# Kernel optimization log

Hardware: AMD Instinct MI355X
Metric: run time of the kernel (lower is better)

The kernel has to match this reference:

```python
import jax, jax.numpy as jnp
import numpy as np

B, T, D, H = 2, 1024, 1024, 16
HS = D // H
EPS = 1e-5
SCALE = float(np.sqrt(HS))  # faithful bug: scores / hs**(-0.5) == scores * sqrt(hs)


def setup_inputs() -> dict:
    key = jax.random.key(0)
    ks = jax.random.split(key, 20)
    n = lambda k, shape: jax.random.normal(k, shape, dtype=jnp.float32) * 0.02
    return {
        "src": jax.random.normal(ks[0], (B, T, D), dtype=jnp.float32),
        "att": jax.random.normal(ks[1], (B, T, D), dtype=jnp.float32),
        # causal masked self-attention (no biases on q/k/v)
        "wq_m": n(ks[2], (H, D, HS)), "wk_m": n(ks[3], (H, D, HS)), "wv_m": n(ks[4], (H, D, HS)),
        "proj_m_w": n(ks[5], (D, D)), "proj_m_b": jnp.zeros((D,), jnp.float32),
        # final (cross) attention (biases on q/k/v)
        "wq_f": n(ks[6], (H, D, HS)), "wk_f": n(ks[7], (H, D, HS)), "wv_f": n(ks[8], (H, D, HS)),
        "bq_f": jnp.zeros((H, HS), jnp.float32), "bk_f": jnp.zeros((H, HS), jnp.float32),
        "bv_f": jnp.zeros((H, HS), jnp.float32),
        "proj_f_w": n(ks[9], (D, D)), "proj_f_b": jnp.zeros((D,), jnp.float32),
        # FFN
        "w1": n(ks[10], (D, 4 * D)), "b1": jnp.zeros((4 * D,), jnp.float32),
        "w2": n(ks[11], (4 * D, D)), "b2": jnp.zeros((D,), jnp.float32),
        # shared RMSNorm weight (one instance reused at all three sites)
        "norm_w": jnp.ones((D,), jnp.float32),
    }


def rmsnorm(x, w):
    return x * jax.lax.rsqrt(jnp.mean(x * x, axis=-1, keepdims=True) + EPS) * w


def masked_attn(x, wq, wk, wv):
    q = jnp.einsum('btd,hde->bhte', x, wq)
    k = jnp.einsum('btd,hde->bhte', x, wk)
    v = jnp.einsum('btd,hde->bhte', x, wv)
    scores = jnp.einsum('bhte,bhse->bhts', q, k) * SCALE  # [B,H,T,T]
    causal = jnp.tril(jnp.ones((T, T), dtype=bool))
    scores = jnp.where(causal, scores, -jnp.inf)
    a = jax.nn.softmax(scores, axis=-1)
    o = jnp.einsum('bhts,bhse->bhte', a, v)
    return o.transpose(0, 2, 1, 3).reshape(B, T, D)  # concat heads


def final_attn(x, att, wq, bq, wk, bk, wv, bv):
    q = jnp.einsum('btd,hde->bhte', att, wq) + bq[None, :, None, :]
    k = jnp.einsum('btd,hde->bhte', att, wk) + bk[None, :, None, :]
    v = jnp.einsum('btd,hde->bhte', x, wv) + bv[None, :, None, :]
    scores = jnp.einsum('bhte,bhse->bhts', q, k) * SCALE
    a = jax.nn.softmax(scores, axis=-1)
    o = jnp.einsum('bhts,bhse->bhte', a, v)
    return o.transpose(0, 2, 1, 3).reshape(B, T, D)


def reference(src, att, wq_m, wk_m, wv_m, proj_m_w, proj_m_b,
              wq_f, wk_f, wv_f, bq_f, bk_f, bv_f, proj_f_w, proj_f_b,
              w1, b1, w2, b2, norm_w):
    # masked self-attention block
    m = masked_attn(rmsnorm(src, norm_w), wq_m, wk_m, wv_m)
    m_out = src + (m @ proj_m_w + proj_m_b)
    # cross attention block (q/k from norm(att), v from m_out)
    f = final_attn(m_out, rmsnorm(att, norm_w), wq_f, bq_f, wk_f, bk_f, wv_f, bv_f)
    f_out = m_out + (f @ proj_f_w + proj_f_b)
    # FFN block
    h = rmsnorm(f_out, norm_w)
    h = jax.nn.gelu(h @ w1 + b1, approximate=False) @ w2 + b2
    return f_out + h
```

## Files before the change

### kernel.cpp

```cpp
#include <hip/hip_runtime.h>
#include <math.h>

#define BB 2
#define TT 1024
#define DD 1024
#define HH 16
#define HS 64
#define NROWS (BB*TT)

typedef _Float16 f16;
typedef __attribute__((ext_vector_type(8))) _Float16 half8;
typedef __attribute__((ext_vector_type(4))) _Float16 half4;
typedef __attribute__((ext_vector_type(4))) float f32x4;

constexpr float EPS   = 1e-5f;
constexpr float SCALE = 8.0f;

__device__ __forceinline__ void load_lds16(const f16* g, f16* l) {
    __builtin_amdgcn_global_load_lds(
        (const __attribute__((address_space(1))) unsigned int*)g,
        (__attribute__((address_space(3))) unsigned int*)l, 16, 0, 0);
}

__device__ __forceinline__ int xcd_swizzle(int lin, int total) {
    if ((total & 7) == 0) {
        const int chunk = total >> 3;
        lin = (lin & 7) * chunk + (lin >> 3);
    }
    return lin;
}

__global__ __launch_bounds__(256) void prologue_all(
    const float* __restrict__ wq_m, const float* __restrict__ wk_m,
    const float* __restrict__ wv_m, const float* __restrict__ proj_m_w,
    const float* __restrict__ wq_f, const float* __restrict__ wk_f,
    const float* __restrict__ wv_f, const float* __restrict__ proj_f_w,
    const float* __restrict__ w1,   const float* __restrict__ w2,
    f16* __restrict__ wt,
    const float* __restrict__ bq, const float* __restrict__ bk,
    float* __restrict__ biascat,
    const float* __restrict__ src, const float* __restrict__ att,
    const float* __restrict__ normw,
    f16* __restrict__ xn_s, f16* __restrict__ xn_a)
{
    const int bid = blockIdx.x;
    const int tid = threadIdx.x;
    const size_t M_ = 1024 * 1024;

    __shared__ float tt[64][65];

    if (bid == 4096) {
        for (int j = tid; j < 5120; j += 256)
            biascat[j] = (j < 3072) ? 0.f : ((j < 4096) ? bq[j - 3072] : bk[j - 4096]);
        return;
    }

    if (bid > 4096) {
        const int rrow = bid - 4097;
        const int row  = rrow & (NROWS - 1);
        const float* xr = ((rrow < NROWS) ? src : att) + (size_t)row * DD;
        f16* out = ((rrow < NROWS) ? xn_s : xn_a) + (size_t)row * DD;

        float4 xv = reinterpret_cast<const float4*>(xr)[tid];
        float ss = xv.x*xv.x + xv.y*xv.y + xv.z*xv.z + xv.w*xv.w;
        float* red = &tt[0][0];
        red[tid] = ss; __syncthreads();
        for (int s = 128; s > 0; s >>= 1) {
            if (tid < s) red[tid] += red[tid + s];
            __syncthreads();
        }
        const float inv = rsqrtf(red[0] * (1.0f / DD) + EPS);
        float4 wv = reinterpret_cast<const float4*>(normw)[tid];
        half4 o;
        o.x = (f16)(xv.x * inv * wv.x);
        o.y = (f16)(xv.y * inv * wv.y);
        o.z = (f16)(xv.z * inv * wv.z);
        o.w = (f16)(xv.w * inv * wv.w);
        *reinterpret_cast<half4*>(&out[tid * 4]) = o;
        return;
    }

    const float* W; f16* Wt; int K, N, lognk, t; bool headw;
    if (bid < 768)       { const int m = bid >> 8;
                           W = (m == 0) ? wq_m : (m == 1) ? wk_m : wv_m;
                           Wt = wt + (size_t)m * M_;
                           K = 1024; N = 1024; lognk = 4; headw = true;  t = bid & 255; }
    else if (bid < 1024) { W = proj_m_w; Wt = wt + 6 * M_;
                           K = 1024; N = 1024; lognk = 4; headw = false; t = bid - 768; }
    else if (bid < 1792) { const int m = (bid - 1024) >> 8;
                           W = (m == 0) ? wq_f : (m == 1) ? wk_f : wv_f;
                           Wt = wt + (size_t)(3 + m) * M_;
                           K = 1024; N = 1024; lognk = 4; headw = true;  t = (bid - 1024) & 255; }
    else if (bid < 2048) { W = proj_f_w; Wt = wt + 7 * M_;
                           K = 1024; N = 1024; lognk = 4; headw = false; t = bid - 1792; }
    else if (bid < 3072) { W = w1; Wt = wt + 8 * M_;
                           K = 1024; N = 4096; lognk = 4; headw = false; t = bid - 2048; }
    else                 { W = w2; Wt = wt + 12 * M_;
                           K = 4096; N = 1024; lognk = 6; headw = false; t = bid - 3072; }

    const int k0 = (t & ((1 << lognk) - 1)) * 64;
    const int n0 = (t >> lognk) * 64;

    #pragma unroll
    for (int r = 0; r < 4; ++r) {
        const int idx = tid + r * 256;
        const int kl  = idx >> 4;
        const int nl4 = (idx & 15) * 4;
        const float* gp;
        if (headw) {
            gp = W + ((size_t)(n0 >> 6) * K + (k0 + kl)) * 64 + nl4;
        } else {
            gp = W + (size_t)(k0 + kl) * N + n0 + nl4;
        }
        float4 v = *reinterpret_cast<const float4*>(gp);
        tt[kl][nl4 + 0] = v.x; tt[kl][nl4 + 1] = v.y;
        tt[kl][nl4 + 2] = v.z; tt[kl][nl4 + 3] = v.w;
    }
    __syncthreads();
    #pragma unroll
    for (int r = 0; r < 4; ++r) {
        const int idx = tid + r * 256;
        const int nl  = idx >> 4;
        const int kl4 = (idx & 15) * 4;
        half4 o;
        o.x = (f16)tt[kl4 + 0][nl];
        o.y = (f16)tt[kl4 + 1][nl];
        o.z = (f16)tt[kl4 + 2][nl];
        o.w = (f16)tt[kl4 + 3][nl];
        *reinterpret_cast<half4*>(&Wt[(size_t)(n0 + nl) * K + k0 + kl4]) = o;
    }
}

template<int BM, int EPI, bool HEADOUT, bool SPLITA, bool OHALF, bool PARTIAL>
__global__ __launch_bounds__(256, 2) void gemm_mfma(
    const f16* __restrict__ A1,
    const f16* __restrict__ A2,
    const f16* __restrict__ Bt,
    const float* __restrict__ bias,
    float* __restrict__ outF,
    f16* __restrict__ outH,
    int N, int K, int splitN)
{
    constexpr int BK = 32;
    constexpr int MI = 4;
    constexpr int NI = (BM == 128) ? 4 : 2;
    constexpr int WN = (BM == 128) ? 64 : 32;
    constexpr int ASLOT = BM * 4;
    constexpr int AINST = ASLOT / 256;

    __shared__ f16 ldsA[2][ASLOT * 8];
    __shared__ f16 ldsB[2][512 * 8];

    const int tid  = threadIdx.x;
    const int lane = tid & 63;
    const int wid  = tid >> 6;
    const int gy = gridDim.y;
    const int lin = xcd_swizzle(blockIdx.y * gridDim.x + blockIdx.x,
                                gridDim.x * gy);
    const int m0 = (lin % gy) * BM;
    const int n0 = (lin / gy) * 128;
    const int wm = (BM == 128) ? (wid >> 1) : 0;
    const int wn = (BM == 128) ? (wid & 1) : wid;

    const int Klen  = K / gridDim.z;
    const int kbase = blockIdx.z * Klen;

    const f16* Aptr = (SPLITA && n0 >= splitN) ? A2 : A1;

    f32x4 acc[MI][NI];
    #pragma unroll
    for (int i = 0; i < MI; ++i)
        #pragma unroll
        for (int j = 0; j < NI; ++j)
            acc[i][j] = (f32x4){0.f, 0.f, 0.f, 0.f};

    auto stage = [&](int buf, int kt) {
        const int k0 = kbase + kt * BK;
        #pragma unroll
        for (int i = 0; i < AINST; ++i) {
            const int s   = (wid * AINST + i) * 64 + lane;
            const int kh  = s / BM;
            const int row = s % BM;
            load_lds16(Aptr + (size_t)(m0 + row) * K + (k0 + kh * 8),
                       &ldsA[buf][s * 8]);
        }
        #pragma unroll
        for (int i = 0; i < 2; ++i) {
            const int s   = (wid * 2 + i) * 64 + lane;
            const int kh  = s >> 7;
            const int col = s & 127;
            load_lds16(Bt + (size_t)(n0 + col) * K + (k0 + kh * 8),
                       &ldsB[buf][s * 8]);
        }
    };

    const int NT = Klen / BK;
    stage(0, 0);
    __syncthreads();
    int cur = 0;
    const int l15 = lane & 15, l4 = lane >> 4;
    for (int kt = 0; kt < NT; ++kt) {
        if (kt + 1 < NT) stage(cur ^ 1, kt + 1);
        half8 af[MI], bfr[NI];
        #pragma unroll
        for (int mi = 0; mi < MI; ++mi)
            af[mi] = *reinterpret_cast<const half8*>(
                &ldsA[cur][(l4 * BM + wm * 64 + mi * 16 + l15) * 8]);
        #pragma unroll
        for (int ni = 0; ni < NI; ++ni)
            bfr[ni] = *reinterpret_cast<const half8*>(
                &ldsB[cur][(l4 * 128 + wn * WN + ni * 16 + l15) * 8]);
        #pragma unroll
        for (int mi = 0; mi < MI; ++mi)
            #pragma unroll
            for (int ni = 0; ni < NI; ++ni)
                acc[mi][ni] = __builtin_amdgcn_mfma_f32_16x16x32_f16(
                    af[mi], bfr[ni], acc[mi][ni], 0, 0, 0);
        __syncthreads();
        cur ^= 1;
    }

    f16* pout = nullptr;
    if (PARTIAL) {
        const size_t MN = (size_t)gridDim.y * BM * N;
        pout = outH + (size_t)blockIdx.z * MN;
    }

    #pragma unroll
    for (int mi = 0; mi < MI; ++mi) {
        #pragma unroll
        for (int ni = 0; ni < NI; ++ni) {
            #pragma unroll
            for (int r = 0; r < 4; ++r) {
                const int row = m0 + wm * 64 + mi * 16 + l4 * 4 + r;
                const int col = n0 + wn * WN + ni * 16 + l15;
                float v = acc[mi][ni][r];
                if (PARTIAL) {
                    pout[(size_t)row * N + col] = (f16)v;
                    continue;
                }
                if (EPI >= 1) v += bias[col];
                if (EPI == 2) v = 0.5f * v * (1.0f + erff(v * 0.70710678118f));
                size_t oidx;
                if (HEADOUT) {
                    const int mat = col >> 10;
                    const int h = (col >> 6) & 15, e = col & 63;
                    const int b = row >> 10, t = row & (TT - 1);
                    oidx = (size_t)mat * ((size_t)NROWS * DD)
                         + ((size_t)((b * HH + h) * TT + t)) * HS + e;
                } else {
                    oidx = (size_t)row * N + col;
                }
                if (OHALF) outH[oidx] = (f16)v;
                else       outF[oidx] = v;
            }
        }
    }
}

template<int MODE>
__global__ __launch_bounds__(256) void reduce_fuse(const f16* __restrict__ part,
                                                   const float* __restrict__ bias,
                                                   const float* __restrict__ residF,
                                                   const f16* __restrict__ residH,
                                                   float* __restrict__ outF,
                                                   f16* __restrict__ outH,
                                                   const float* __restrict__ normw,
                                                   f16* __restrict__ xnout) {
    const size_t MN  = (size_t)NROWS * 1024;
    const int tid = threadIdx.x;
    const size_t idx = ((size_t)blockIdx.x * 256 + tid) * 4;
    float o[4];
    {
        half4 p0 = *reinterpret_cast<const half4*>(part + idx);
        half4 p1 = *reinterpret_cast<const half4*>(part + MN + idx);
        half4 p2 = *reinterpret_cast<const half4*>(part + 2 * MN + idx);
        half4 p3 = *reinterpret_cast<const half4*>(part + 3 * MN + idx);
        float4 bi = *reinterpret_cast<const float4*>(bias + (idx & 1023));
        o[0] = (float)p0.x + (float)p1.x + (float)p2.x + (float)p3.x + bi.x;
        o[1] = (float)p0.y + (float)p1.y + (float)p2.y + (float)p3.y + bi.y;
        o[2] = (float)p0.z + (float)p1.z + (float)p2.z + (float)p3.z + bi.z;
        o[3] = (float)p0.w + (float)p1.w + (float)p2.w + (float)p3.w + bi.w;
    }
    if (MODE == 0 || MODE == 2) {
        float4 rs = *reinterpret_cast<const float4*>(residF + idx);
        o[0] += rs.x; o[1] += rs.y; o[2] += rs.z; o[3] += rs.w;
    } else {
        half4 rh = *reinterpret_cast<const half4*>(residH + idx);
        o[0] += (float)rh.x; o[1] += (float)rh.y; o[2] += (float)rh.z; o[3] += (float)rh.w;
    }

    if (MODE == 0) {
        half4 h;
        h.x = (f16)o[0]; h.y = (f16)o[1]; h.z = (f16)o[2]; h.w = (f16)o[3];
        *reinterpret_cast<half4*>(outH + idx) = h;
        return;
    }

    float4 ov = {o[0], o[1], o[2], o[3]};
    *reinterpret_cast<float4*>(outF + idx) = ov;

    if (MODE == 1) {
        __shared__ float red[256];
        red[tid] = o[0]*o[0] + o[1]*o[1] + o[2]*o[2] + o[3]*o[3];
        __syncthreads();
        for (int s = 128; s > 0; s >>= 1) {
            if (tid < s) red[tid] += red[tid + s];
            __syncthreads();
        }
        const float inv = rsqrtf(red[0] * (1.0f / DD) + EPS);
        float4 nw = *reinterpret_cast<const float4*>(normw + (idx & 1023));
        half4 h;
        h.x = (f16)(o[0] * inv * nw.x);
        h.y = (f16)(o[1] * inv * nw.y);
        h.z = (f16)(o[2] * inv * nw.z);
        h.w = (f16)(o[3] * inv * nw.w);
        *reinterpret_cast<half4*>(xnout + idx) = h;
    }
}

__global__ __launch_bounds__(256) void reduce_vf(const f16* __restrict__ part,
                                                 const float* __restrict__ bv,
                                                 f16* __restrict__ out) {
    const size_t MN = (size_t)NROWS * 1024;
    const int t   = blockIdx.x;
    const int tid = threadIdx.x;
    const int n   = tid * 4;
    const size_t idx = (size_t)t * 1024 + n;
    half4 p0 = *reinterpret_cast<const half4*>(part + idx);
    half4 p1 = *reinterpret_cast<const half4*>(part + MN + idx);
    float4 bi = *reinterpret_cast<const float4*>(bv + n);
    half4 o;
    o.x = (f16)((float)p0.x + (float)p1.x + bi.x);
    o.y = (f16)((float)p0.y + (float)p1.y + bi.y);
    o.z = (f16)((float)p0.z + (float)p1.z + bi.z);
    o.w = (f16)((float)p0.w + (float)p1.w + bi.w);
    const int b = t >> 10, tl = t & (TT - 1);
    const int h = n >> 6, e = n & (HS - 1);
    *reinterpret_cast<half4*>(
        &out[((size_t)(b * HH + h) * TT + tl) * HS + e]) = o;
}

template<bool CAUSAL>
__global__ __launch_bounds__(256) void attn_mfma(const f16* __restrict__ Q,
                                                 const f16* __restrict__ Kg,
                                                 const f16* __restrict__ Vg,
                                                 f16* __restrict__ O) {
    int iq, bh;
    if (CAUSAL) {
        bh = blockIdx.y;
        iq = (blockIdx.y < 16) ? blockIdx.x : (15 - blockIdx.x);
    } else {
        iq = blockIdx.x; bh = blockIdx.y;
    }
    const int tid = threadIdx.x;
    const int lane = tid & 63;
    const int w   = tid >> 6;
    const int l15 = lane & 15, l4 = lane >> 4;

    __shared__ f16 Ks[512 * 8];
    __shared__ f16 VT[64 * 72];
    __shared__ f16 Ps[4][16 * 72];

    const f16* qb = Q  + ((size_t)bh * TT + (size_t)iq * 64) * HS;
    const f16* kb = Kg + (size_t)bh * TT * HS;
    const f16* vb = Vg + (size_t)bh * TT * HS;

    half8 qf[2];
    #pragma unroll
    for (int ks = 0; ks < 2; ++ks)
        qf[ks] = *reinterpret_cast<const half8*>(
            qb + (size_t)(w * 16 + l15) * HS + ks * 32 + l4 * 8);

    f32x4 oacc[4];
    #pragma unroll
    for (int ni = 0; ni < 4; ++ni) oacc[ni] = (f32x4){0.f, 0.f, 0.f, 0.f};
    float m_run[4], l_run[4];
    #pragma unroll
    for (int r = 0; r < 4; ++r) { m_run[r] = -1e30f; l_run[r] = 0.f; }

    const int sp  = lane & 31;
    const int ehv = lane >> 5;
    const int c0  = w * 16 + ehv * 8;

    const int ntiles = CAUSAL ? (iq + 1) : (TT / 64);
    for (int js = 0; js < ntiles; ++js) {
        __syncthreads();

        #pragma unroll
        for (int i = 0; i < 2; ++i) {
            const int slot = (w * 2 + i) * 64 + lane;
            load_lds16(kb + (size_t)(js * 64 + (slot & 63)) * HS + (slot >> 6) * 8,
                       &Ks[slot * 8]);
        }
        {
            const f16* vrow = vb + (size_t)(js * 64 + 2 * sp) * HS + c0;
            uint4 r0 = *reinterpret_cast<const uint4*>(vrow);
            uint4 r1 = *reinterpret_cast<const uint4*>(vrow + HS);
            const unsigned rc0[4] = {r0.x, r0.y, r0.z, r0.w};
            const unsigned rc1[4] = {r1.x, r1.y, r1.z, r1.w};
            #pragma unroll
            for (int i = 0; i < 8; ++i) {
                const unsigned lo = (i & 1) ? (rc0[i >> 1] >> 16) : (rc0[i >> 1] & 0xffffu);
                const unsigned hi = (i & 1) ? (rc1[i >> 1] >> 16) : (rc1[i >> 1] & 0xffffu);
                *reinterpret_cast<unsigned*>(&VT[(c0 + i) * 72 + 2 * sp]) = lo | (hi << 16);
            }
        }
        __syncthreads();

        f32x4 sacc[4];
        #pragma unroll
        for (int ni = 0; ni < 4; ++ni) sacc[ni] = (f32x4){0.f, 0.f, 0.f, 0.f};
        __builtin_amdgcn_s_setprio(1);
        #pragma unroll
        for (int ks = 0; ks < 2; ++ks) {
            #pragma unroll
            for (int ni = 0; ni < 4; ++ni) {
                half8 kf = *reinterpret_cast<const half8*>(
                    &Ks[((ks * 4 + l4) * 64 + ni * 16 + l15) * 8]);
                sacc[ni] = __builtin_amdgcn_mfma_f32_16x16x32_f16(qf[ks], kf, sacc[ni], 0, 0, 0);
            }
        }
        __builtin_amdgcn_s_setprio(0);

        float sv[4][4];
        #pragma unroll
        for (int ni = 0; ni < 4; ++ni) {
            #pragma unroll
            for (int r = 0; r < 4; ++r) {
                float x = sacc[ni][r] * SCALE;
                if (CAUSAL && js == iq) {
                    const int sg = js * 64 + ni * 16 + l15;
                    const int qg = iq * 64 + w * 16 + l4 * 4 + r;
                    if (sg > qg) x = -1e30f;
                }
                sv[ni][r] = x;
            }
        }

        #pragma unroll
        for (int r = 0; r < 4; ++r) {
            float rm = fmaxf(fmaxf(sv[0][r], sv[1][r]), fmaxf(sv[2][r], sv[3][r]));
            rm = fmaxf(rm, __shfl_xor(rm, 1));
            rm = fmaxf(rm, __shfl_xor(rm, 2));
            rm = fmaxf(rm, __shfl_xor(rm, 4));
            rm = fmaxf(rm, __shfl_xor(rm, 8));
            const float mnew = fmaxf(m_run[r], rm);
            const float corr = __expf(m_run[r] - mnew);
            float p0 = __expf(sv[0][r] - mnew);
            float p1 = __expf(sv[1][r] - mnew);
            float p2 = __expf(sv[2][r] - mnew);
            float p3 = __expf(sv[3][r] - mnew);
            float sum = p0 + p1 + p2 + p3;
            sum += __shfl_xor(sum, 1);
            sum += __shfl_xor(sum, 2);
            sum += __shfl_xor(sum, 4);
            sum += __shfl_xor(sum, 8);
            l_run[r] = l_run[r] * corr + sum;
            m_run[r] = mnew;
            #pragma unroll
            for (int ni = 0; ni < 4; ++ni) oacc[ni][r] *= corr;
            f16* prow = &Ps[w][(l4 * 4 + r) * 72];
            prow[ 0 + l15] = (f16)p0;
            prow[16 + l15] = (f16)p1;
            prow[32 + l15] = (f16)p2;
            prow[48 + l15] = (f16)p3;
        }

        __builtin_amdgcn_s_setprio(1);
        #pragma unroll
        for (int ks = 0; ks < 2; ++ks) {
            half8 pf = *reinterpret_cast<const half8*>(&Ps[w][l15 * 72 + ks * 32 + l4 * 8]);
            #pragma unroll
            for (int ni = 0; ni < 4; ++ni) {
                half8 vf = *reinterpret_cast<const half8*>(
                    &VT[(ni * 16 + l15) * 72 + ks * 32 + l4 * 8]);
                oacc[ni] = __builtin_amdgcn_mfma_f32_16x16x32_f16(pf, vf, oacc[ni], 0, 0, 0);
            }
        }
        __builtin_amdgcn_s_setprio(0);
    }

    const int b = bh >> 4, h = bh & (HH - 1);
    #pragma unroll
    for (int r = 0; r < 4; ++r) {
        const float inv = 1.0f / l_run[r];
        const int t = iq * 64 + w * 16 + l4 * 4 + r;
        #pragma unroll
        for (int ni = 0; ni < 4; ++ni)
            O[((size_t)(b * TT + t)) * DD + h * HS + ni * 16 + l15] =
                (f16)(oacc[ni][r] * inv);
    }
}

extern "C" void kernel_launch(void* const* d_in, const int* in_sizes, int n_in,
                              void* d_out, int out_size, void* d_ws, size_t ws_size,
                              hipStream_t stream) {
    const float* src      = (const float*)d_in[0];
    const float* att      = (const float*)d_in[1];
    const float* wq_m     = (const float*)d_in[2];
    const float* wk_m     = (const float*)d_in[3];
    const float* wv_m     = (const float*)d_in[4];
    const float* proj_m_w = (const float*)d_in[5];
    const float* proj_m_b = (const float*)d_in[6];
    const float* wq_f     = (const float*)d_in[7];
    const float* wk_f     = (const float*)d_in[8];
    const float* wv_f     = (const float*)d_in[9];
    const float* bq_f     = (const float*)d_in[10];
    const float* bk_f     = (const float*)d_in[11];
    const float* bv_f     = (const float*)d_in[12];
    const float* proj_f_w = (const float*)d_in[13];
    const float* proj_f_b = (const float*)d_in[14];
    const float* w1       = (const float*)d_in[15];
    const float* b1       = (const float*)d_in[16];
    const float* w2       = (const float*)d_in[17];
    const float* b2       = (const float*)d_in[18];
    const float* norm_w   = (const float*)d_in[19];

    const size_t M_ = 1024 * 1024;
    f16* wsb = (f16*)d_ws;
    f16* wt      = wsb;
    f16* headbuf = wsb + 16 * M_;
    f16* h1      = wsb + 16 * M_;
    f16* xn_s    = wsb + 28 * M_;
    f16* xn_a    = wsb + 30 * M_;
    f16* ao      = wsb + 32 * M_;
    f16* mo_h    = wsb + 34 * M_;
    f16* partH   = wsb + 36 * M_;
    f16* xn2     = wsb + 44 * M_;
    float* biascat = (float*)d_out;
    float* f_out = (float*)d_out;
    float* outp  = (float*)d_out;
    (void)ws_size; (void)in_sizes; (void)n_in;

    const dim3 blk(256);
    const int BIG = 1 << 30;
    const dim3 gQKV(40, 16);
    const dim3 gVF(8, 32, 2);
    const dim3 gW1(32, 16);
    const dim3 gSPLIT(8, 16, 4);
    const dim3 gRED(2048);

    prologue_all<<<dim3(8193), blk, 0, stream>>>(
        wq_m, wk_m, wv_m, proj_m_w, wq_f, wk_f, wv_f, proj_f_w, w1, w2,
        wt, bq_f, bk_f, biascat, src, att, norm_w, xn_s, xn_a);

    gemm_mfma<128, 1, true, true, true, false><<<gQKV, blk, 0, stream>>>(
        xn_s, xn_a, wt, biascat, nullptr, headbuf, 5120, 1024, 3072);

    attn_mfma<true><<<dim3(16, 32), blk, 0, stream>>>(
        headbuf, headbuf + 2 * M_, headbuf + 4 * M_, ao);
    gemm_mfma<128, 0, false, false, false, true><<<gSPLIT, blk, 0, stream>>>(
        ao, nullptr, wt + 6 * M_, nullptr, nullptr, partH, 1024, 1024, BIG);
    reduce_fuse<0><<<gRED, blk, 0, stream>>>(
        partH, proj_m_b, src, nullptr, nullptr, mo_h, nullptr, nullptr);

    gemm_mfma<64, 0, false, false, false, true><<<gVF, blk, 0, stream>>>(
        mo_h, nullptr, wt + 5 * M_, nullptr, nullptr, partH, 1024, 1024, BIG);
    reduce_vf<<<dim3(NROWS), blk, 0, stream>>>(partH, bv_f, headbuf + 10 * M_);
    attn_mfma<false><<<dim3(16, 32), blk, 0, stream>>>(
        headbuf + 6 * M_, headbuf + 8 * M_, headbuf + 10 * M_, ao);
    gemm_mfma<128, 0, false, false, false, true><<<gSPLIT, blk, 0, stream>>>(
        ao, nullptr, wt + 7 * M_, nullptr, nullptr, partH, 1024, 1024, BIG);
    reduce_fuse<1><<<gRED, blk, 0, stream>>>(
        partH, proj_f_b, nullptr, mo_h, f_out, nullptr, norm_w, xn2);

    gemm_mfma<128, 2, false, false, true, false><<<gW1, blk, 0, stream>>>(
        xn2, nullptr, wt + 8 * M_, b1, nullptr, h1, 4096, 1024, BIG);
    gemm_mfma<128, 0, false, false, false, true><<<gSPLIT, blk, 0, stream>>>(
        h1, nullptr, wt + 12 * M_, nullptr, nullptr, partH, 1024, 4096, BIG);
    reduce_fuse<2><<<gRED, blk, 0, stream>>>(
        partH, b2, f_out, nullptr, outp, nullptr, nullptr, nullptr);
}
```

Baseline: 295.7 us.

## Double-buffer K/V tiles in attention kernel to overlap loads with compute

Attention K and transposed V tiles now live in two LDS buffers. The next tile's K is staged asynchronously and its V rows are loaded into registers while the current tile's QK^T and softmax run. V is packed into the alternate buffer before the PV MFMA, so there is one barrier per iteration instead of two. The cost is double the LDS for K/V and more live registers, which may reduce occupancy. The attention kernel is only part of a larger pipeline that also contains large GEMMs.

```diff
diff --git a/kernel.cpp b/kernel.cpp
--- a/kernel.cpp
+++ b/kernel.cpp
@@ -358,8 +358,8 @@
     const int w   = tid >> 6;
     const int l15 = lane & 15, l4 = lane >> 4;
 
-    __shared__ f16 Ks[512 * 8];
-    __shared__ f16 VT[64 * 72];
+    __shared__ f16 Ks[2][512 * 8];
+    __shared__ f16 VT[2][64 * 72];
     __shared__ f16 Ps[4][16 * 72];
 
     const f16* qb = Q  + ((size_t)bh * TT + (size_t)iq * 64) * HS;
@@ -383,30 +383,48 @@
     const int ehv = lane >> 5;
     const int c0  = w * 16 + ehv * 8;
 
-    const int ntiles = CAUSAL ? (iq + 1) : (TT / 64);
-    for (int js = 0; js < ntiles; ++js) {
-        __syncthreads();
-
+    auto stageK = [&](int buf, int js) {
         #pragma unroll
         for (int i = 0; i < 2; ++i) {
             const int slot = (w * 2 + i) * 64 + lane;
             load_lds16(kb + (size_t)(js * 64 + (slot & 63)) * HS + (slot >> 6) * 8,
-                       &Ks[slot * 8]);
-        }
-        {
-            const f16* vrow = vb + (size_t)(js * 64 + 2 * sp) * HS + c0;
-            uint4 r0 = *reinterpret_cast<const uint4*>(vrow);
-            uint4 r1 = *reinterpret_cast<const uint4*>(vrow + HS);
-            const unsigned rc0[4] = {r0.x, r0.y, r0.z, r0.w};
-            const unsigned rc1[4] = {r1.x, r1.y, r1.z, r1.w};
-            #pragma unroll
-            for (int i = 0; i < 8; ++i) {
-                const unsigned lo = (i & 1) ? (rc0[i >> 1] >> 16) : (rc0[i >> 1] & 0xffffu);
-                const unsigned hi = (i & 1) ? (rc1[i >> 1] >> 16) : (rc1[i >> 1] & 0xffffu);
-                *reinterpret_cast<unsigned*>(&VT[(c0 + i) * 72 + 2 * sp]) = lo | (hi << 16);
-            }
-        }
-        __syncthreads();
+                       &Ks[buf][slot * 8]);
+        }
+    };
+    auto loadV = [&](int js, uint4& r0, uint4& r1) {
+        const f16* vrow = vb + (size_t)(js * 64 + 2 * sp) * HS + c0;
+        r0 = *reinterpret_cast<const uint4*>(vrow);
+        r1 = *reinterpret_cast<const uint4*>(vrow + HS);
+    };
+    auto packV = [&](int buf, const uint4& r0, const uint4& r1) {
+        const unsigned rc0[4] = {r0.x, r0.y, r0.z, r0.w};
+        const unsigned rc1[4] = {r1.x, r1.y, r1.z, r1.w};
+        #pragma unroll
+        for (int i = 0; i < 8; ++i) {
+            const unsigned lo = (i & 1) ? (rc0[i >> 1] >> 16) : (rc0[i >> 1] & 0xffffu);
+            const unsigned hi = (i & 1) ? (rc1[i >> 1] >> 16) : (rc1[i >> 1] & 0xffffu);
+            *reinterpret_cast<unsigned*>(&VT[buf][(c0 + i) * 72 + 2 * sp]) = lo | (hi << 16);
+        }
+    };
+
+    const int ntiles = CAUSAL ? (iq + 1) : (TT / 64);
+
+    {
+        uint4 v0, v1;
+        stageK(0, 0);
+        loadV(0, v0, v1);
+        packV(0, v0, v1);
+    }
+    __syncthreads();
+
+    int cur = 0;
+    for (int js = 0; js < ntiles; ++js) {
+        const bool has_next = (js + 1 < ntiles);
+        uint4 v0, v1;
+        if (has_next) {
+            stageK(cur ^ 1, js + 1);
+            loadV(js + 1, v0, v1);
+        }
 
         f32x4 sacc[4];
         #pragma unroll
@@ -417,7 +435,7 @@
             #pragma unroll
             for (int ni = 0; ni < 4; ++ni) {
                 half8 kf = *reinterpret_cast<const half8*>(
-                    &Ks[((ks * 4 + l4) * 64 + ni * 16 + l15) * 8]);
+                    &Ks[cur][((ks * 4 + l4) * 64 + ni * 16 + l15) * 8]);
                 sacc[ni] = __builtin_amdgcn_mfma_f32_16x16x32_f16(qf[ks], kf, sacc[ni], 0, 0, 0);
             }
         }
@@ -467,6 +485,8 @@
             prow[48 + l15] = (f16)p3;
         }
 
+        if (has_next) packV(cur ^ 1, v0, v1);
+
         __builtin_amdgcn_s_setprio(1);
         #pragma unroll
         for (int ks = 0; ks < 2; ++ks) {
@@ -474,11 +494,14 @@
             #pragma unroll
             for (int ni = 0; ni < 4; ++ni) {
                 half8 vf = *reinterpret_cast<const half8*>(
-                    &VT[(ni * 16 + l15) * 72 + ks * 32 + l4 * 8]);
+                    &VT[cur][(ni * 16 + l15) * 72 + ks * 32 + l4 * 8]);
                 oacc[ni] = __builtin_amdgcn_mfma_f32_16x16x32_f16(pf, vf, oacc[ni], 0, 0, 0);
             }
         }
         __builtin_amdgcn_s_setprio(0);
+
+        __syncthreads();
+        cur ^= 1;
     }
 
     const int b = bh >> 4, h = bh & (HH - 1);
```

Result: no change. 294.7 us (median of 3 runs) (-0.3%).
